# Kernel tuning notes

Measured on AMD Instinct MI355X. Metric: run time of the kernel, lower is better.

## Reference

```python
import jax, jax.numpy as jnp
import numpy as np

B, N, D, H, DK, DV, E = 32, 512, 128, 8, 16, 16, 128
MLP_H = 16


def _uniform(key, shape, fan):
    s = 1.0 / np.sqrt(fan)
    return jax.random.uniform(key, shape, jnp.float32, -s, s)


def setup_inputs() -> dict:
    key = jax.random.key(0)
    ks = jax.random.split(key, 13)
    q = jax.random.normal(ks[0], (B, N, D), jnp.float32)
    mask = jax.random.randint(ks[1], (B, N, N), 0, 2) > 0  # True = attention not allowed
    edge_matrix = jax.random.normal(ks[2], (B, N, N), jnp.float32)
    # per-head projection weights (init: uniform(-1/sqrt(last_dim), ...))
    W_query = _uniform(ks[3], (H, D, DK), DK)
    W_key = _uniform(ks[4], (H, D, DK), DK)
    W_val = _uniform(ks[5], (H, D, DV), DV)
    W_out = _uniform(ks[6], (H, DV, E), E)
    # edge MLP: 1 -> 16 -> 16 -> n_heads, ReLU between layers
    mlp_W1 = _uniform(ks[7], (1, MLP_H), 1)
    mlp_b1 = _uniform(ks[8], (MLP_H,), 1)
    mlp_W2 = _uniform(ks[9], (MLP_H, MLP_H), MLP_H)
    mlp_b2 = _uniform(ks[10], (MLP_H,), MLP_H)
    mlp_W3 = _uniform(ks[11], (MLP_H, H), MLP_H)
    mlp_b3 = _uniform(ks[12], (H,), MLP_H)
    return dict(q=q, mask=mask, edge_matrix=edge_matrix,
                W_query=W_query, W_key=W_key, W_val=W_val, W_out=W_out,
                mlp_W1=mlp_W1, mlp_b1=mlp_b1, mlp_W2=mlp_W2, mlp_b2=mlp_b2,
                mlp_W3=mlp_W3, mlp_b3=mlp_b3)


def reference(q, mask, edge_matrix, W_query, W_key, W_val, W_out,
              mlp_W1, mlp_b1, mlp_W2, mlp_b2, mlp_W3, mlp_b3):
    dk = W_query.shape[-1]
    norm = 1.0 / np.sqrt(dk)
    # per-head projections: [H,B,N,dk]
    Q = jnp.einsum('bni,hid->hbnd', q, W_query)
    K = jnp.einsum('bni,hid->hbnd', q, W_key)
    V = jnp.einsum('bni,hid->hbnd', q, W_val)
    # scaled QK^T: [H,B,N,N]
    comp = norm * jnp.einsum('hbqd,hbkd->hbqk', Q, K)
    # edge-bias MLP on each scalar edge weight: [B,N,N,1] -> [B,N,N,H]
    e = edge_matrix[..., None]
    h1 = jax.nn.relu(e @ mlp_W1 + mlp_b1)
    h2 = jax.nn.relu(h1 @ mlp_W2 + mlp_b2)
    bias = h2 @ mlp_W3 + mlp_b3
    comp = comp + jnp.transpose(bias, (3, 0, 1, 2))
    # masked softmax (mask True = disallowed)
    m = mask[None]  # broadcast over heads
    comp = jnp.where(m, -jnp.inf, comp)
    attn = jax.nn.softmax(comp, axis=-1)
    attn = jnp.where(m, 0.0, attn)
    heads = jnp.einsum('hbqk,hbkd->hbqd', attn, V)  # [H,B,N,dv]
    out = jnp.einsum('hbqd,hde->bqe', heads, W_out)  # [B,N,E]
    return out
```

## Files before the change

### kernel.cpp

```cpp
#include <hip/hip_runtime.h>
#include <hip/hip_bf16.h>
#include <float.h>

#define Bc 32
#define Nc 512
#define Dc 128
#define Hc 8
#define DKc 16
#define Ec 128
#define LOG2E 1.44269504088896340736f
#define SCLAMP 80.0f
#define KPAD 3.0e38f

typedef __attribute__((ext_vector_type(4))) short s16x4;
typedef __attribute__((ext_vector_type(8))) short s16x8;
typedef __attribute__((ext_vector_type(4))) float f32x4;

union BFU { __hip_bfloat16 b; short s; };
static __device__ inline short f2bf(float f) { BFU u; u.b = __float2bfloat16(f); return u.s; }
static __device__ inline s16x4 pack4(float a, float b, float c, float d) {
  s16x4 r; r[0] = f2bf(a); r[1] = f2bf(b); r[2] = f2bf(c); r[3] = f2bf(d); return r;
}

#if __has_builtin(__builtin_amdgcn_exp2f)
#define EXP2F(x) __builtin_amdgcn_exp2f(x)
#else
#define EXP2F(x) exp2f(x)
#endif

static __device__ inline f32x4 mfma16(s16x4 a, s16x4 b, f32x4 c) {
#if __has_builtin(__builtin_amdgcn_mfma_f32_16x16x16bf16_1k)
  return __builtin_amdgcn_mfma_f32_16x16x16bf16_1k(a, b, c, 0, 0, 0);
#else
  int lane = threadIdx.x & 63;
  int g = lane >> 4, base = lane & 15;
  int src0 = (base + 32 * g) & 63;
  int src1 = (base + 32 * g + 16) & 63;
  int ax = ((int*)&a)[0], ay = ((int*)&a)[1];
  int bx = ((int*)&b)[0], by = ((int*)&b)[1];
  int A0 = __shfl(ax, src0), A1 = __shfl(ay, src0);
  int A2 = __shfl(ax, src1), A3 = __shfl(ay, src1);
  int B0 = __shfl(bx, src0), B1 = __shfl(by, src0);
  int B2 = __shfl(bx, src1), B3 = __shfl(by, src1);
  if (g >= 2) { A0 = A1 = A2 = A3 = 0; B0 = B1 = B2 = B3 = 0; }
  s16x8 A8, B8;
  ((int*)&A8)[0] = A0; ((int*)&A8)[1] = A1; ((int*)&A8)[2] = A2; ((int*)&A8)[3] = A3;
  ((int*)&B8)[0] = B0; ((int*)&B8)[1] = B1; ((int*)&B8)[2] = B2; ((int*)&B8)[3] = B3;
  return __builtin_amdgcn_mfma_f32_16x16x32_bf16(A8, B8, c, 0, 0, 0);
#endif
}

static __device__ __forceinline__ void h2pre_eval(
    float e, const float* W1, const float* B1, const float* W2, const float* B2,
    float* h2)
{
  float h1[16];
  #pragma unroll
  for (int u = 0; u < 16; ++u) h1[u] = fmaxf(0.f, fmaf(e, W1[u], B1[u]));
  #pragma unroll
  for (int v = 0; v < 16; ++v) {
    float a = B2[v];
    #pragma unroll
    for (int u = 0; u < 16; ++u) a = fmaf(h1[u], W2[u * 16 + v], a);
    h2[v] = a;
  }
}
static __device__ __forceinline__ void bias_eval(
    float e, const float* W1, const float* B1, const float* W2, const float* B2,
    const float* W3, const float* B3, float* bias8)
{
  float h2[16];
  h2pre_eval(e, W1, B1, W2, B2, h2);
  #pragma unroll
  for (int h = 0; h < 8; ++h) {
    float a = B3[h];
    #pragma unroll
    for (int v = 0; v < 16; ++v) a = fmaf(fmaxf(h2[v], 0.f), W3[v * 8 + h], a);
    bias8[h] = a;
  }
}

__global__ __launch_bounds__(256) void prep_kernel(
    const float* __restrict__ Wq, const float* __restrict__ Wk, const float* __restrict__ Wv,
    const float* __restrict__ Wo,
    const unsigned char* __restrict__ m, int* __restrict__ flag,
    short* __restrict__ Wt, short* __restrict__ Wob,
    const float* __restrict__ mW1, const float* __restrict__ mb1,
    const float* __restrict__ mW2, const float* __restrict__ mb2,
    const float* __restrict__ mW3, const float* __restrict__ mb3,
    float* __restrict__ knotsG, float* __restrict__ coeffG)
{
  int blk = blockIdx.x;
  int t = threadIdx.x;

  if (blk == 256) {
    __shared__ int red[4];
    int any = 0;
    for (int u = t; u < 16384; u += 256)
      if ((u & 3) != 0 && m[u] != 0) any = 1;
    unsigned long long bal = __ballot(any != 0);
    if ((t & 63) == 0) red[t >> 6] = (bal != 0ULL) ? 1 : 0;
    __syncthreads();
    if (t == 0) *flag = red[0] | red[1] | red[2] | red[3];
    return;
  }

  if (blk == 257) {
    __shared__ float t1raw[16], t1s[16];
    __shared__ float ks[512], ks2[512];
    __shared__ int cnt, n1s;

    if (t < 16) {
      float w = mW1[t];
      t1raw[t] = (w != 0.f) ? (-mb1[t] / w) : KPAD;
    }
    for (int u = t; u < 512; u += 256) { ks[u] = KPAD; ks2[u] = KPAD; }
    __syncthreads();
    if (t < 16) {
      float v = t1raw[t];
      int r = 0;
      #pragma unroll
      for (int j = 0; j < 16; ++j) {
        float vj = t1raw[j];
        r += (vj < v) || (vj == v && j < t);
      }
      t1s[r] = v;
    }
    __syncthreads();
    if (t == 0) {
      int n1 = 0;
      while (n1 < 16 && t1s[n1] < 1.0e37f) { ks[n1] = t1s[n1]; n1++; }
      n1s = n1;
      cnt = n1;
    }
    __syncthreads();
    int n1 = n1s;
    if (t <= n1) {
      bool first = (t == 0), last = (t == n1);
      float L = first ? 0.f : t1s[t - 1];
      float R = last ? 0.f : t1s[t];
      float p1, p2;
      bool ok = true;
      if (first && last) { p1 = 0.f; p2 = 1.f; }
      else if (first)    { p1 = R - 1.f; p2 = R - 0.5f; }
      else if (last)     { p1 = L + 0.5f; p2 = L + 1.f; }
      else {
        float w = R - L;
        if (w > 0.f) { p1 = L + 0.25f * w; p2 = L + 0.75f * w; }
        else ok = false;
      }
      if (ok && p2 > p1) {
        float h2a[16], h2b[16];
        h2pre_eval(p1, mW1, mb1, mW2, mb2, h2a);
        h2pre_eval(p2, mW1, mb1, mW2, mb2, h2b);
        #pragma unroll
        for (int v = 0; v < 16; ++v) {
          float bet = (h2b[v] - h2a[v]) / (p2 - p1);
          float alp = fmaf(-bet, p1, h2a[v]);
          float x = -alp / bet;
          bool fin = (x == x) && (fabsf(x) < 1.0e37f) && (bet != 0.f);
          bool inr = (first || x > L) && (last || x < R);
          if (fin && inr) { int id = atomicAdd(&cnt, 1); ks[id] = x; }
        }
      }
    }
    __syncthreads();
    int mknots = cnt;
    for (int i = t; i < mknots; i += 256) {
      float v = ks[i];
      int r = 0;
      for (int j = 0; j < mknots; ++j) {
        float vj = ks[j];
        r += (vj < v) || (vj == v && j < i);
      }
      ks2[r] = v;
    }
    __syncthreads();
    for (int u = t; u < 512; u += 256) knotsG[u] = ks2[u];
    for (int s = t; s < mknots + 1; s += 256) {
      bool first = (s == 0), last = (s == mknots);
      float L = first ? 0.f : ks2[s - 1];
      float R = last ? 0.f : ks2[s];
      float p1, p2;
      if (first && last) { p1 = 0.f; p2 = 1.f; }
      else if (first)    { p1 = R - 1.f; p2 = R - 0.5f; }
      else if (last)     { p1 = L + 0.5f; p2 = L + 1.f; }
      else { float w = R - L; p1 = L + 0.25f * w; p2 = L + 0.75f * w; }
      float ba[8];
      bias_eval(p1, mW1, mb1, mW2, mb2, mW3, mb3, ba);
      if (p2 > p1) {
        float bb[8];
        bias_eval(p2, mW1, mb1, mW2, mb2, mW3, mb3, bb);
        #pragma unroll
        for (int h = 0; h < 8; ++h) {
          float sl = (bb[h] - ba[h]) / (p2 - p1);
          float c0 = fmaf(-sl, p1, ba[h]);
          coeffG[h * 640 + s * 2]     = sl * LOG2E;
          coeffG[h * 640 + s * 2 + 1] = c0 * LOG2E;
        }
      } else {
        #pragma unroll
        for (int h = 0; h < 8; ++h) {
          coeffG[h * 640 + s * 2]     = 0.f;
          coeffG[h * 640 + s * 2 + 1] = ba[h] * LOG2E;
        }
      }
    }
    return;
  }

  int o = blk * 256 + t;
  if (o < 49152) {
    int mat = o >> 14, r = o & 16383;
    int hk = r >> 7, d = r & 127;
    const float* src = (mat == 0) ? Wq : ((mat == 1) ? Wk : Wv);
    Wt[o] = f2bf(src[(hk >> 4) * 2048 + d * 16 + (hk & 15)]);
  } else {
    int o2 = o - 49152;
    int et = o2 >> 11, s = (o2 >> 8) & 7, lane = (o2 >> 2) & 63, i = o2 & 3;
    Wob[o2] = f2bf(Wo[(s * 16 + (lane >> 4) * 4 + i) * 128 + et * 16 + (lane & 15)]);
  }
}

__global__ __launch_bounds__(256, 4) void qkv4(
    const float* __restrict__ q, const short* __restrict__ Wt,
    short* __restrict__ Qb, short* __restrict__ Kb, short* __restrict__ Vt)
{
  __shared__ short qs[16][136];
  int blk = blockIdx.x;
  int b = blk >> 5;
  int rt = (blk & 31) << 4;
  int t = threadIdx.x;
  int wid = t >> 6, lane = t & 63;
  int lq = lane & 15, lg = lane >> 4;

  #pragma unroll
  for (int it = 0; it < 2; ++it) {
    int u = t + it * 256;
    int row = u >> 5, c4 = (u & 31) << 2;
    float4 v = *(const float4*)&q[((((b << 9) + rt + row) << 7)) + c4];
    *(s16x4*)&qs[row][c4] = pack4(v.x, v.y, v.z, v.w);
  }
  __syncthreads();

  s16x4 af[8];
  #pragma unroll
  for (int ks = 0; ks < 8; ++ks)
    af[ks] = *(const s16x4*)&qs[lq][ks * 16 + lg * 4];

  #pragma unroll 1
  for (int pj = 0; pj < 3; ++pj) {
    const short* Wm = Wt + pj * 16384;
    #pragma unroll
    for (int c2 = 0; c2 < 2; ++c2) {
      int ct = wid * 2 + c2;
      f32x4 acc = (f32x4)0.f;
      #pragma unroll
      for (int ks = 0; ks < 8; ++ks) {
        s16x4 bf = *(const s16x4*)&Wm[(ct * 16 + lq) * 128 + ks * 16 + lg * 4];
        acc = mfma16(af[ks], bf, acc);
      }
      if (pj == 0) {
        s16x4 pk = pack4(acc[0] * (0.25f * LOG2E), acc[1] * (0.25f * LOG2E),
                         acc[2] * (0.25f * LOG2E), acc[3] * (0.25f * LOG2E));
        #pragma unroll
        for (int r = 0; r < 4; ++r)
          Qb[(ct << 18) + (b << 13) + ((rt + lg * 4 + r) << 4) + lq] = pk[r];
      } else if (pj == 1) {
        s16x4 pk = pack4(acc[0], acc[1], acc[2], acc[3]);
        #pragma unroll
        for (int r = 0; r < 4; ++r)
          Kb[(ct << 18) + (b << 13) + ((rt + lg * 4 + r) << 4) + lq] = pk[r];
      } else {
        s16x4 pk = pack4(acc[0], acc[1], acc[2], acc[3]);
        *(s16x4*)&Vt[(ct << 18) + (((b << 4) + lq) << 9) + rt + lg * 4] = pk;
      }
    }
  }
}

static __device__ __forceinline__ int segof(const float* knotsL, float e) {
  int p = 0;
  #pragma unroll
  for (int s = 256; s > 0; s >>= 1)
    p += (knotsL[p + s - 1] <= e) ? s : 0;
  return p;
}

__global__ __launch_bounds__(256, 4) void attn7(
    const float* __restrict__ edge, const unsigned char* __restrict__ maskB,
    const int* __restrict__ flag,
    const short* __restrict__ Qb, const short* __restrict__ Kb, const short* __restrict__ Vt,
    const short* __restrict__ Wob,
    const float* __restrict__ knotsG, const float* __restrict__ coeffG,
    float* __restrict__ out)
{
  __shared__ __align__(16) char smem[36864];

  int t = threadIdx.x;
  int wid = t >> 6, lane = t & 63;
  int lq = lane & 15, lg = lane >> 4;
  int b = blockIdx.x >> 5;
  int qt = (blockIdx.x & 31) << 4;
  int mflag = *flag;

  float* knotsL = (float*)smem;
  float* coeffL = (float*)(smem + 2048);
  float* d2L = (float*)smem;
  float* psL = (float*)(smem + 34816);

  for (int u = t; u < 1408; u += 256)
    ((float4*)smem)[u] = ((const float4*)knotsG)[u];

  const short* Kl = Kb + (b << 13) + (lq << 4) + (lg << 2);
  const short* Vl = Vt + (((b << 4) + lq) << 9) + (lg << 2);
  const short* Ql = Qb + (b << 13) + ((qt + lq) << 4) + (lg << 2);
  unsigned mbase = (((b << 9) + qt + lq) << 9) + (lg << 2);

  s16x4 qf[8];
  #pragma unroll
  for (int h = 0; h < 8; ++h) qf[h] = *(const s16x4*)(Ql + (h << 18));

  f32x4 oacc[8];
  float psum[8];
  #pragma unroll
  for (int h = 0; h < 8; ++h) { oacc[h] = (f32x4)0.f; psum[h] = 0.f; }

  int jb = wid << 4;
  float4 ev = *(const float4*)&edge[mbase + jb];
  int4 mkv;
  if (mflag) {
    uchar4 u = *(const uchar4*)&maskB[mbase + jb];
    mkv.x = u.x; mkv.y = u.y; mkv.z = u.z; mkv.w = u.w;
  } else {
    mkv = *(const int4*)&((const int*)maskB)[mbase + jb];
  }

  __syncthreads();

  #pragma unroll 1
  for (int cc = 0; cc < 8; ++cc) {
    jb = ((cc << 2) | wid) << 4;

    float4 evn; int4 mkn;
    if (cc < 7) {
      int jbn = (((cc + 1) << 2) | wid) << 4;
      evn = *(const float4*)&edge[mbase + jbn];
      if (mflag) {
        uchar4 u = *(const uchar4*)&maskB[mbase + jbn];
        mkn.x = u.x; mkn.y = u.y; mkn.z = u.z; mkn.w = u.w;
      } else {
        mkn = *(const int4*)&((const int*)maskB)[mbase + jbn];
      }
    } else { evn = ev; mkn = mkv; }

    s16x4 kf[8];
    #pragma unroll
    for (int h = 0; h < 8; ++h) kf[h] = *(const s16x4*)(Kl + (h << 18) + (jb << 4));

    int sg0 = segof(knotsL, ev.x);
    int sg1 = segof(knotsL, ev.y);
    int sg2 = segof(knotsL, ev.z);
    int sg3 = segof(knotsL, ev.w);
    const float* c0 = coeffL + (sg0 << 1);
    const float* c1 = coeffL + (sg1 << 1);
    const float* c2 = coeffL + (sg2 << 1);
    const float* c3 = coeffL + (sg3 << 1);

    #pragma unroll
    for (int h = 0; h < 8; ++h) {
      int hb = h * 640;
      float2 a0 = *(const float2*)(c0 + hb);
      float2 a1 = *(const float2*)(c1 + hb);
      float2 a2 = *(const float2*)(c2 + hb);
      float2 a3 = *(const float2*)(c3 + hb);
      f32x4 sc;
      sc[0] = fmaf(a0.x, ev.x, a0.y);
      sc[1] = fmaf(a1.x, ev.y, a1.y);
      sc[2] = fmaf(a2.x, ev.z, a2.y);
      sc[3] = fmaf(a3.x, ev.w, a3.y);
      sc = mfma16(kf[h], qf[h], sc);
      s16x4 vf = *(const s16x4*)(Vl + (h << 18) + jb);
      float p0 = mkv.x ? 0.f : EXP2F(fminf(sc[0], SCLAMP));
      float p1 = mkv.y ? 0.f : EXP2F(fminf(sc[1], SCLAMP));
      float p2 = mkv.z ? 0.f : EXP2F(fminf(sc[2], SCLAMP));
      float p3 = mkv.w ? 0.f : EXP2F(fminf(sc[3], SCLAMP));
      psum[h] += (p0 + p1) + (p2 + p3);
      s16x4 pf = pack4(p0, p1, p2, p3);
      oacc[h] = mfma16(vf, pf, oacc[h]);
    }
    ev = evn; mkv = mkn;
  }

  #pragma unroll
  for (int h = 0; h < 8; ++h) {
    float s = psum[h];
    s += __shfl_xor(s, 16);
    s += __shfl_xor(s, 32);
    psum[h] = s;
  }
  if (lg == 0) {
    #pragma unroll
    for (int h = 0; h < 8; ++h) psL[wid * 128 + h * 16 + lq] = psum[h];
  }
  __syncthreads();

  s16x4 obf[8];
  #pragma unroll
  for (int h = 0; h < 8; ++h) {
    float tot = psL[h * 16 + lq] + psL[128 + h * 16 + lq]
              + psL[256 + h * 16 + lq] + psL[384 + h * 16 + lq];
    float inv = (tot > 0.f) ? 1.f / tot : 0.f;
    obf[h] = pack4(oacc[h][0] * inv, oacc[h][1] * inv, oacc[h][2] * inv, oacc[h][3] * inv);
  }

  f32x4 d2a[8];
  #pragma unroll
  for (int et = 0; et < 8; ++et) d2a[et] = (f32x4)0.f;
  #pragma unroll
  for (int s = 0; s < 8; ++s) {
    #pragma unroll
    for (int et = 0; et < 8; ++et) {
      s16x4 wo = *(const s16x4*)&Wob[((et * 8 + s) << 8) + (lane << 2)];
      d2a[et] = mfma16(wo, obf[s], d2a[et]);
    }
  }

  #pragma unroll
  for (int et = 0; et < 8; ++et)
    #pragma unroll
    for (int r = 0; r < 4; ++r)
      d2L[(wid * 128 + et * 16 + lg * 4 + r) * 17 + lq] = d2a[et][r];
  __syncthreads();

  #pragma unroll
  for (int k = 0; k < 2; ++k) {
    int et = wid * 2 + k;
    #pragma unroll
    for (int r = 0; r < 4; ++r) {
      int el = (et * 16 + lg * 4 + r) * 17 + lq;
      float v = d2L[el] + d2L[2176 + el] + d2L[4352 + el] + d2L[6528 + el];
      out[(((b << 9) + qt + lq) << 7) + et * 16 + lg * 4 + r] = v;
    }
  }
}

extern "C" void kernel_launch(void* const* d_in, const int* in_sizes, int n_in,
                              void* d_out, int out_size, void* d_ws, size_t ws_size,
                              hipStream_t stream)
{
  const float* q    = (const float*)d_in[0];
  const unsigned char* mask = (const unsigned char*)d_in[1];
  const float* edge = (const float*)d_in[2];
  const float* Wq   = (const float*)d_in[3];
  const float* Wk   = (const float*)d_in[4];
  const float* Wv   = (const float*)d_in[5];
  const float* Wo   = (const float*)d_in[6];
  const float* mW1  = (const float*)d_in[7];
  const float* mb1  = (const float*)d_in[8];
  const float* mW2  = (const float*)d_in[9];
  const float* mb2  = (const float*)d_in[10];
  const float* mW3  = (const float*)d_in[11];
  const float* mb3  = (const float*)d_in[12];
  float* out = (float*)d_out;

  size_t per = (size_t)Hc * Bc * Nc * DKc;
  short* Wt  = (short*)d_ws;
  short* Wob = Wt + 49152;
  short* Qb  = Wob + 16384;
  short* Kb  = Qb + per;
  short* Vt  = Kb + per;
  float* knotsG = (float*)(Vt + per);
  float* coeffG = knotsG + 512;
  int* flag  = (int*)(coeffG + 5120);

  prep_kernel<<<dim3(258), dim3(256), 0, stream>>>(Wq, Wk, Wv, Wo, mask, flag, Wt, Wob,
      mW1, mb1, mW2, mb2, mW3, mb3, knotsG, coeffG);
  qkv4<<<dim3(Bc * 32), dim3(256), 0, stream>>>(q, Wt, Qb, Kb, Vt);
  attn7<<<dim3(Bc * 32), dim3(256), 0, stream>>>(edge, mask, flag, Qb, Kb, Vt, Wob,
      knotsG, coeffG, out);
}
```

Before: 141.6 us.

## Replace binary knot search with two-level segment lookup and interleaved coeff table

Moves the piecewise-linear edge-MLP table construction into its own single-block kernel. The knots are now stored hierarchically: first-layer ReLU breakpoints, then per-interval second-layer crossings. The attention kernel replaces its 9-step dependent binary search over 512 knots with a branch-free count over 16 register-held breakpoints plus 16 crossings loaded as vectors. It also computes next-chunk segments one iteration ahead, and coefficients are laid out per segment with all heads contiguous so one 16-byte load serves two heads. This adds an extra tiny kernel launch and more compare instructions per edge, in exchange for fewer dependent LDS accesses.

```diff
diff --git a/kernel.cpp b/kernel.cpp
--- a/kernel.cpp
+++ b/kernel.cpp
@@ -50,49 +50,38 @@
 #endif
 }
 
-static __device__ __forceinline__ void h2pre_eval(
-    float e, const float* W1, const float* B1, const float* W2, const float* B2,
-    float* h2)
-{
+static __device__ __forceinline__ void h2pre_eval(float e, const float* wl, float* h2) {
   float h1[16];
   #pragma unroll
-  for (int u = 0; u < 16; ++u) h1[u] = fmaxf(0.f, fmaf(e, W1[u], B1[u]));
+  for (int u = 0; u < 16; ++u) h1[u] = fmaxf(0.f, fmaf(e, wl[u], wl[16 + u]));
   #pragma unroll
   for (int v = 0; v < 16; ++v) {
-    float a = B2[v];
-    #pragma unroll
-    for (int u = 0; u < 16; ++u) a = fmaf(h1[u], W2[u * 16 + v], a);
+    float a = wl[288 + v];
+    #pragma unroll
+    for (int u = 0; u < 16; ++u) a = fmaf(h1[u], wl[32 + u * 16 + v], a);
     h2[v] = a;
   }
 }
-static __device__ __forceinline__ void bias_eval(
-    float e, const float* W1, const float* B1, const float* W2, const float* B2,
-    const float* W3, const float* B3, float* bias8)
-{
+static __device__ __forceinline__ void bias_eval(float e, const float* wl, float* b8) {
   float h2[16];
-  h2pre_eval(e, W1, B1, W2, B2, h2);
+  h2pre_eval(e, wl, h2);
   #pragma unroll
   for (int h = 0; h < 8; ++h) {
-    float a = B3[h];
-    #pragma unroll
-    for (int v = 0; v < 16; ++v) a = fmaf(fmaxf(h2[v], 0.f), W3[v * 8 + h], a);
-    bias8[h] = a;
-  }
-}
-
-__global__ __launch_bounds__(256) void prep_kernel(
+    float a = wl[432 + h];
+    #pragma unroll
+    for (int v = 0; v < 16; ++v) a = fmaf(fmaxf(h2[v], 0.f), wl[304 + v * 8 + h], a);
+    b8[h] = a;
+  }
+}
+
+__global__ __launch_bounds__(256) void prep_conv(
     const float* __restrict__ Wq, const float* __restrict__ Wk, const float* __restrict__ Wv,
     const float* __restrict__ Wo,
     const unsigned char* __restrict__ m, int* __restrict__ flag,
-    short* __restrict__ Wt, short* __restrict__ Wob,
-    const float* __restrict__ mW1, const float* __restrict__ mb1,
-    const float* __restrict__ mW2, const float* __restrict__ mb2,
-    const float* __restrict__ mW3, const float* __restrict__ mb3,
-    float* __restrict__ knotsG, float* __restrict__ coeffG)
+    short* __restrict__ Wt, short* __restrict__ Wob)
 {
   int blk = blockIdx.x;
   int t = threadIdx.x;
-
   if (blk == 256) {
     __shared__ int red[4];
     int any = 0;
@@ -104,111 +93,6 @@
     if (t == 0) *flag = red[0] | red[1] | red[2] | red[3];
     return;
   }
-
-  if (blk == 257) {
-    __shared__ float t1raw[16], t1s[16];
-    __shared__ float ks[512], ks2[512];
-    __shared__ int cnt, n1s;
-
-    if (t < 16) {
-      float w = mW1[t];
-      t1raw[t] = (w != 0.f) ? (-mb1[t] / w) : KPAD;
-    }
-    for (int u = t; u < 512; u += 256) { ks[u] = KPAD; ks2[u] = KPAD; }
-    __syncthreads();
-    if (t < 16) {
-      float v = t1raw[t];
-      int r = 0;
-      #pragma unroll
-      for (int j = 0; j < 16; ++j) {
-        float vj = t1raw[j];
-        r += (vj < v) || (vj == v && j < t);
-      }
-      t1s[r] = v;
-    }
-    __syncthreads();
-    if (t == 0) {
-      int n1 = 0;
-      while (n1 < 16 && t1s[n1] < 1.0e37f) { ks[n1] = t1s[n1]; n1++; }
-      n1s = n1;
-      cnt = n1;
-    }
-    __syncthreads();
-    int n1 = n1s;
-    if (t <= n1) {
-      bool first = (t == 0), last = (t == n1);
-      float L = first ? 0.f : t1s[t - 1];
-      float R = last ? 0.f : t1s[t];
-      float p1, p2;
-      bool ok = true;
-      if (first && last) { p1 = 0.f; p2 = 1.f; }
-      else if (first)    { p1 = R - 1.f; p2 = R - 0.5f; }
-      else if (last)     { p1 = L + 0.5f; p2 = L + 1.f; }
-      else {
-        float w = R - L;
-        if (w > 0.f) { p1 = L + 0.25f * w; p2 = L + 0.75f * w; }
-        else ok = false;
-      }
-      if (ok && p2 > p1) {
-        float h2a[16], h2b[16];
-        h2pre_eval(p1, mW1, mb1, mW2, mb2, h2a);
-        h2pre_eval(p2, mW1, mb1, mW2, mb2, h2b);
-        #pragma unroll
-        for (int v = 0; v < 16; ++v) {
-          float bet = (h2b[v] - h2a[v]) / (p2 - p1);
-          float alp = fmaf(-bet, p1, h2a[v]);
-          float x = -alp / bet;
-          bool fin = (x == x) && (fabsf(x) < 1.0e37f) && (bet != 0.f);
-          bool inr = (first || x > L) && (last || x < R);
-          if (fin && inr) { int id = atomicAdd(&cnt, 1); ks[id] = x; }
-        }
-      }
-    }
-    __syncthreads();
-    int mknots = cnt;
-    for (int i = t; i < mknots; i += 256) {
-      float v = ks[i];
-      int r = 0;
-      for (int j = 0; j < mknots; ++j) {
-        float vj = ks[j];
-        r += (vj < v) || (vj == v && j < i);
-      }
-      ks2[r] = v;
-    }
-    __syncthreads();
-    for (int u = t; u < 512; u += 256) knotsG[u] = ks2[u];
-    for (int s = t; s < mknots + 1; s += 256) {
-      bool first = (s == 0), last = (s == mknots);
-      float L = first ? 0.f : ks2[s - 1];
-      float R = last ? 0.f : ks2[s];
-      float p1, p2;
-      if (first && last) { p1 = 0.f; p2 = 1.f; }
-      else if (first)    { p1 = R - 1.f; p2 = R - 0.5f; }
-      else if (last)     { p1 = L + 0.5f; p2 = L + 1.f; }
-      else { float w = R - L; p1 = L + 0.25f * w; p2 = L + 0.75f * w; }
-      float ba[8];
-      bias_eval(p1, mW1, mb1, mW2, mb2, mW3, mb3, ba);
-      if (p2 > p1) {
-        float bb[8];
-        bias_eval(p2, mW1, mb1, mW2, mb2, mW3, mb3, bb);
-        #pragma unroll
-        for (int h = 0; h < 8; ++h) {
-          float sl = (bb[h] - ba[h]) / (p2 - p1);
-          float c0 = fmaf(-sl, p1, ba[h]);
-          coeffG[h * 640 + s * 2]     = sl * LOG2E;
-          coeffG[h * 640 + s * 2 + 1] = c0 * LOG2E;
-        }
-      } else {
-        #pragma unroll
-        for (int h = 0; h < 8; ++h) {
-          coeffG[h * 640 + s * 2]     = 0.f;
-          coeffG[h * 640 + s * 2 + 1] = ba[h] * LOG2E;
-        }
-      }
-    }
-    return;
-  }
-
   int o = blk * 256 + t;
   if (o < 49152) {
     int mat = o >> 14, r = o & 16383;
@@ -219,6 +103,142 @@
     int o2 = o - 49152;
     int et = o2 >> 11, s = (o2 >> 8) & 7, lane = (o2 >> 2) & 63, i = o2 & 3;
     Wob[o2] = f2bf(Wo[(s * 16 + (lane >> 4) * 4 + i) * 128 + et * 16 + (lane & 15)]);
+  }
+}
+
+__global__ __launch_bounds__(64) void tablegen(
+    const float* __restrict__ mW1, const float* __restrict__ mb1,
+    const float* __restrict__ mW2, const float* __restrict__ mb2,
+    const float* __restrict__ mW3, const float* __restrict__ mb3,
+    float* __restrict__ t1G, int* __restrict__ baseG,
+    float* __restrict__ crossG, float* __restrict__ coeffG)
+{
+  __shared__ float wl[440];
+  __shared__ float t1r[16], t1s[16];
+  __shared__ float crs[17][16], crs2[17][16];
+  __shared__ int cnt[17], cums[18];
+  __shared__ float gl[320];
+  __shared__ int n1s, mtots;
+  int t = threadIdx.x;
+
+  for (int u = t; u < 440; u += 64) {
+    float v;
+    if (u < 16) v = mW1[u];
+    else if (u < 32)  v = mb1[u - 16];
+    else if (u < 288) v = mW2[u - 32];
+    else if (u < 304) v = mb2[u - 288];
+    else if (u < 432) v = mW3[u - 304];
+    else v = mb3[u - 432];
+    wl[u] = v;
+  }
+  for (int u = t; u < 272; u += 64) { ((float*)crs)[u] = KPAD; ((float*)crs2)[u] = KPAD; }
+  for (int u = t; u < 320; u += 64) gl[u] = KPAD;
+  if (t < 17) cnt[t] = 0;
+  __syncthreads();
+  if (t < 16) { float w = wl[t]; t1r[t] = (w != 0.f) ? (-wl[16 + t] / w) : KPAD; }
+  __syncthreads();
+  if (t < 16) {
+    float v = t1r[t]; int r = 0;
+    #pragma unroll
+    for (int j = 0; j < 16; ++j) { float vj = t1r[j]; r += (vj < v) || (vj == v && j < t); }
+    t1s[r] = v;
+  }
+  __syncthreads();
+  if (t == 0) { int n = 0; while (n < 16 && t1s[n] < 1.0e37f) n++; n1s = n; }
+  __syncthreads();
+  int n1 = n1s;
+
+  if (t <= n1) {
+    bool first = (t == 0), last = (t == n1);
+    float L = first ? 0.f : t1s[t - 1];
+    float R = last ? 0.f : t1s[t];
+    float p1 = 0.f, p2 = 0.f; bool ok = true;
+    if (first && last)      { p1 = 0.f; p2 = 1.f; }
+    else if (first)         { p1 = R - 1.f; p2 = R - 0.5f; }
+    else if (last)          { p1 = L + 0.5f; p2 = L + 1.f; }
+    else { float w = R - L; if (w > 0.f) { p1 = L + 0.25f * w; p2 = L + 0.75f * w; } else ok = false; }
+    if (ok) {
+      float h2a[16], h2b[16];
+      h2pre_eval(p1, wl, h2a);
+      h2pre_eval(p2, wl, h2b);
+      int k = 0;
+      #pragma unroll
+      for (int v = 0; v < 16; ++v) {
+        float bet = (h2b[v] - h2a[v]) / (p2 - p1);
+        float alp = fmaf(-bet, p1, h2a[v]);
+        float x = -alp / bet;
+        bool fin = (x == x) && (fabsf(x) < 1.0e37f) && (bet != 0.f);
+        bool inr = (first || x > L) && (last || x < R);
+        if (fin && inr) { crs[t][k] = x; k++; }
+      }
+      cnt[t] = k;
+    }
+  }
+  __syncthreads();
+
+  {
+    float vv[5]; int rr[5]; int nn = 0;
+    for (int u = t; u < 272; u += 64) {
+      int i = u >> 4, j = u & 15;
+      float v = crs[i][j];
+      if (v < 1.0e37f) {
+        int r = 0;
+        #pragma unroll
+        for (int j2 = 0; j2 < 16; ++j2) { float v2 = crs[i][j2]; r += (v2 < v) || (v2 == v && j2 < j); }
+        vv[nn] = v; rr[nn] = (i << 4) + r; nn++;
+      }
+    }
+    __syncthreads();
+    for (int m2 = 0; m2 < nn; ++m2) ((float*)crs2)[rr[m2]] = vv[m2];
+  }
+  __syncthreads();
+  if (t == 0) {
+    int c = 0; cums[0] = 0;
+    for (int i = 0; i < 17; ++i) { c += cnt[i]; cums[i + 1] = c; }
+    mtots = n1 + cums[n1 + 1];
+  }
+  __syncthreads();
+  int mtot = mtots;
+
+  if (t < n1) gl[cums[t + 1] + t] = t1s[t];
+  if (t <= n1) {
+    int base = cums[t] + t;
+    for (int j = 0; j < cnt[t]; ++j) gl[base + j] = crs2[t][j];
+  }
+  __syncthreads();
+
+  if (t < 16) t1G[t] = t1s[t];
+  if (t < 32) baseG[t] = (t < 17) ? (t + cums[t]) : 0;
+  for (int u = t; u < 272; u += 64) crossG[u] = ((float*)crs2)[u];
+
+  for (int s = t; s <= mtot; s += 64) {
+    bool first = (s == 0), last = (s == mtot);
+    float L = first ? 0.f : gl[s - 1];
+    float R = last ? 0.f : gl[s];
+    float p1, p2;
+    if (first && last)      { p1 = 0.f; p2 = 1.f; }
+    else if (first)         { p1 = R - 1.f; p2 = R - 0.5f; }
+    else if (last)          { p1 = L + 0.5f; p2 = L + 1.f; }
+    else { float w = R - L; p1 = L + 0.25f * w; p2 = L + 0.75f * w; }
+    float ba[8];
+    bias_eval(p1, wl, ba);
+    if (p2 > p1) {
+      float bb[8];
+      bias_eval(p2, wl, bb);
+      #pragma unroll
+      for (int h = 0; h < 8; ++h) {
+        float sl = (bb[h] - ba[h]) / (p2 - p1);
+        float c0 = fmaf(-sl, p1, ba[h]);
+        coeffG[s * 16 + h * 2]     = sl * LOG2E;
+        coeffG[s * 16 + h * 2 + 1] = c0 * LOG2E;
+      }
+    } else {
+      #pragma unroll
+      for (int h = 0; h < 8; ++h) {
+        coeffG[s * 16 + h * 2]     = 0.f;
+        coeffG[s * 16 + h * 2 + 1] = ba[h] * LOG2E;
+      }
+    }
   }
 }
 
@@ -279,20 +299,30 @@
   }
 }
 
-static __device__ __forceinline__ int segof(const float* knotsL, float e) {
-  int p = 0;
-  #pragma unroll
-  for (int s = 256; s > 0; s >>= 1)
-    p += (knotsL[p + s - 1] <= e) ? s : 0;
-  return p;
-}
-
-__global__ __launch_bounds__(256, 4) void attn7(
+static __device__ __forceinline__ int seg_lookup(float e, const float* t1c,
+    const int* baseL, const float* crossL)
+{
+  int i1 = 0;
+  #pragma unroll
+  for (int i = 0; i < 16; ++i) i1 += (t1c[i] <= e) ? 1 : 0;
+  int bse = baseL[i1];
+  const f32x4* crp = (const f32x4*)(crossL + (i1 << 4));
+  f32x4 c0 = crp[0], c1 = crp[1], c2 = crp[2], c3 = crp[3];
+  int loc = 0;
+  #pragma unroll
+  for (int k = 0; k < 4; ++k) {
+    loc += (c0[k] <= e); loc += (c1[k] <= e);
+    loc += (c2[k] <= e); loc += (c3[k] <= e);
+  }
+  return bse + loc;
+}
+
+__global__ __launch_bounds__(256, 4) void attn8(
     const float* __restrict__ edge, const unsigned char* __restrict__ maskB,
     const int* __restrict__ flag,
     const short* __restrict__ Qb, const short* __restrict__ Kb, const short* __restrict__ Vt,
     const short* __restrict__ Wob,
-    const float* __restrict__ knotsG, const float* __restrict__ coeffG,
+    const float* __restrict__ t1G, const int* __restrict__ baseG,
     float* __restrict__ out)
 {
   __shared__ __align__(16) char smem[36864];
@@ -304,13 +334,19 @@
   int qt = (blockIdx.x & 31) << 4;
   int mflag = *flag;
 
-  float* knotsL = (float*)smem;
-  float* coeffL = (float*)(smem + 2048);
+  int* baseL = (int*)smem;
+  float* crossL = (float*)(smem + 128);
+  float* coeffL = (float*)(smem + 1216);
   float* d2L = (float*)smem;
   float* psL = (float*)(smem + 34816);
 
-  for (int u = t; u < 1408; u += 256)
-    ((float4*)smem)[u] = ((const float4*)knotsG)[u];
+  for (int u = t; u < 1356; u += 256)
+    ((float4*)smem)[u] = ((const float4*)baseG)[u];
+
+  float t1c[16];
+  #pragma unroll
+  for (int i = 0; i < 16; ++i)
+    t1c[i] = __uint_as_float(__builtin_amdgcn_readfirstlane(__float_as_uint(t1G[i])));
 
   const short* Kl = Kb + (b << 13) + (lq << 4) + (lg << 2);
   const short* Vl = Vt + (((b << 4) + lq) << 9) + (lg << 2);
@@ -337,6 +373,12 @@
   }
 
   __syncthreads();
+
+  int4 sgv;
+  sgv.x = seg_lookup(ev.x, t1c, baseL, crossL);
+  sgv.y = seg_lookup(ev.y, t1c, baseL, crossL);
+  sgv.z = seg_lookup(ev.z, t1c, baseL, crossL);
+  sgv.w = seg_lookup(ev.w, t1c, baseL, crossL);
 
   #pragma unroll 1
   for (int cc = 0; cc < 8; ++cc) {
@@ -358,38 +400,38 @@
     #pragma unroll
     for (int h = 0; h < 8; ++h) kf[h] = *(const s16x4*)(Kl + (h << 18) + (jb << 4));
 
-    int sg0 = segof(knotsL, ev.x);
-    int sg1 = segof(knotsL, ev.y);
-    int sg2 = segof(knotsL, ev.z);
-    int sg3 = segof(knotsL, ev.w);
-    const float* c0 = coeffL + (sg0 << 1);
-    const float* c1 = coeffL + (sg1 << 1);
-    const float* c2 = coeffL + (sg2 << 1);
-    const float* c3 = coeffL + (sg3 << 1);
-
-    #pragma unroll
-    for (int h = 0; h < 8; ++h) {
-      int hb = h * 640;
-      float2 a0 = *(const float2*)(c0 + hb);
-      float2 a1 = *(const float2*)(c1 + hb);
-      float2 a2 = *(const float2*)(c2 + hb);
-      float2 a3 = *(const float2*)(c3 + hb);
-      f32x4 sc;
-      sc[0] = fmaf(a0.x, ev.x, a0.y);
-      sc[1] = fmaf(a1.x, ev.y, a1.y);
-      sc[2] = fmaf(a2.x, ev.z, a2.y);
-      sc[3] = fmaf(a3.x, ev.w, a3.y);
-      sc = mfma16(kf[h], qf[h], sc);
-      s16x4 vf = *(const s16x4*)(Vl + (h << 18) + jb);
-      float p0 = mkv.x ? 0.f : EXP2F(fminf(sc[0], SCLAMP));
-      float p1 = mkv.y ? 0.f : EXP2F(fminf(sc[1], SCLAMP));
-      float p2 = mkv.z ? 0.f : EXP2F(fminf(sc[2], SCLAMP));
-      float p3 = mkv.w ? 0.f : EXP2F(fminf(sc[3], SCLAMP));
-      psum[h] += (p0 + p1) + (p2 + p3);
-      s16x4 pf = pack4(p0, p1, p2, p3);
-      oacc[h] = mfma16(vf, pf, oacc[h]);
-    }
-    ev = evn; mkv = mkn;
+    int4 sgn;
+    sgn.x = seg_lookup(evn.x, t1c, baseL, crossL);
+    sgn.y = seg_lookup(evn.y, t1c, baseL, crossL);
+    sgn.z = seg_lookup(evn.z, t1c, baseL, crossL);
+    sgn.w = seg_lookup(evn.w, t1c, baseL, crossL);
+
+    #pragma unroll
+    for (int hp = 0; hp < 4; ++hp) {
+      f32x4 cx = *(const f32x4*)(coeffL + (sgv.x << 4) + (hp << 2));
+      f32x4 cy = *(const f32x4*)(coeffL + (sgv.y << 4) + (hp << 2));
+      f32x4 cz = *(const f32x4*)(coeffL + (sgv.z << 4) + (hp << 2));
+      f32x4 cw = *(const f32x4*)(coeffL + (sgv.w << 4) + (hp << 2));
+      #pragma unroll
+      for (int hh = 0; hh < 2; ++hh) {
+        int h = hp * 2 + hh;
+        f32x4 sc;
+        sc[0] = fmaf(cx[hh * 2], ev.x, cx[hh * 2 + 1]);
+        sc[1] = fmaf(cy[hh * 2], ev.y, cy[hh * 2 + 1]);
+        sc[2] = fmaf(cz[hh * 2], ev.z, cz[hh * 2 + 1]);
+        sc[3] = fmaf(cw[hh * 2], ev.w, cw[hh * 2 + 1]);
+        sc = mfma16(kf[h], qf[h], sc);
+        s16x4 vf = *(const s16x4*)(Vl + (h << 18) + jb);
+        float p0 = mkv.x ? 0.f : EXP2F(fminf(sc[0], SCLAMP));
+        float p1 = mkv.y ? 0.f : EXP2F(fminf(sc[1], SCLAMP));
+        float p2 = mkv.z ? 0.f : EXP2F(fminf(sc[2], SCLAMP));
+        float p3 = mkv.w ? 0.f : EXP2F(fminf(sc[3], SCLAMP));
+        psum[h] += (p0 + p1) + (p2 + p3);
+        s16x4 pf = pack4(p0, p1, p2, p3);
+        oacc[h] = mfma16(vf, pf, oacc[h]);
+      }
+    }
+    ev = evn; mkv = mkn; sgv = sgn;
   }
 
   #pragma unroll
@@ -470,13 +512,16 @@
   short* Qb  = Wob + 16384;
   short* Kb  = Qb + per;
   short* Vt  = Kb + per;
-  float* knotsG = (float*)(Vt + per);
-  float* coeffG = knotsG + 512;
+  float* t1G = (float*)(Vt + per);
+  int* baseG = (int*)(t1G + 16);
+  float* crossG = (float*)(baseG + 32);
+  float* coeffG = crossG + 272;
   int* flag  = (int*)(coeffG + 5120);
 
-  prep_kernel<<<dim3(258), dim3(256), 0, stream>>>(Wq, Wk, Wv, Wo, mask, flag, Wt, Wob,
-      mW1, mb1, mW2, mb2, mW3, mb3, knotsG, coeffG);
+  prep_conv<<<dim3(257), dim3(256), 0, stream>>>(Wq, Wk, Wv, Wo, mask, flag, Wt, Wob);
+  tablegen<<<dim3(1), dim3(64), 0, stream>>>(mW1, mb1, mW2, mb2, mW3, mb3,
+      t1G, baseG, crossG, coeffG);
   qkv4<<<dim3(Bc * 32), dim3(256), 0, stream>>>(q, Wt, Qb, Kb, Vt);
-  attn7<<<dim3(Bc * 32), dim3(256), 0, stream>>>(edge, mask, flag, Qb, Kb, Vt, Wob,
-      knotsG, coeffG, out);
-}
+  attn8<<<dim3(Bc * 32), dim3(256), 0, stream>>>(edge, mask, flag, Qb, Kb, Vt, Wob,
+      t1G, baseG, out);
+}
```

Measured after the change: 149.4 us. 1.06x slower.
